# Optimization experiments

Measured on AMD Instinct MI355X. Metric: run time of the kernel, lower is better.

## Reference

```python
import jax, jax.numpy as jnp
import numpy as np

# Hyperparameters (must match init_kwargs)
B, S, D = 1, 4096, 1024
H, DK, DV = 16, 64, 64
G, W, R = 1, 23, 8          # global, window, random tokens
KSEL = 1 + R + W            # selected keys per non-global query


def setup_inputs() -> dict:
    key = jax.random.key(0)
    ks = jax.random.split(key, 8)
    scale = 0.02
    Q = jax.random.normal(ks[0], (B, S, D), dtype=jnp.float32)
    K = jax.random.normal(ks[1], (B, S, D), dtype=jnp.float32)
    V = jax.random.normal(ks[2], (B, S, D), dtype=jnp.float32)
    Wq = jax.random.normal(ks[3], (D, H * DK), dtype=jnp.float32) * scale
    Wk = jax.random.normal(ks[4], (D, H * DK), dtype=jnp.float32) * scale
    Wv = jax.random.normal(ks[5], (D, H * DV), dtype=jnp.float32) * scale
    Wo = jax.random.normal(ks[6], (H * DV, D), dtype=jnp.float32) * scale
    # BigBird-style index table: [global(=token 0), random, sliding window]
    n_ng = S - 2 * G
    base = jnp.arange(G, S - G)                                   # [n_ng]
    win = base[:, None] + jnp.arange(W)[None, :] - (W - 1) // 2   # [n_ng, W]
    win = jnp.clip(win, 0, S - 1)
    rnd = jax.random.randint(ks[7], (n_ng, R), 1, S)              # [n_ng, R]
    glb = jnp.zeros((n_ng, 1), dtype=jnp.int64)
    idx = jnp.concatenate([glb, rnd.astype(jnp.int64), win.astype(jnp.int64)], axis=1)  # [n_ng, KSEL]
    return {"Q": Q, "K": K, "V": V, "Wq": Wq, "Wk": Wk, "Wv": Wv, "Wo": Wo, "idx": idx}


def reference(Q, K, V, Wq, Wk, Wv, Wo, idx):
    b, s, _ = Q.shape
    g = G
    # Projections, split heads: [B,H,S,d]
    q = (Q @ Wq).reshape(b, s, H, DK).transpose(0, 2, 1, 3)
    k = (K @ Wk).reshape(b, s, H, DK).transpose(0, 2, 1, 3)
    v = (V @ Wv).reshape(b, s, H, DV).transpose(0, 2, 1, 3)
    scale = 1.0 / jnp.sqrt(jnp.asarray(DK, dtype=q.dtype))

    # --- dense global-token path: first g and last g queries attend to all keys ---
    gidx = jnp.concatenate([jnp.arange(g), jnp.arange(s - g, s)])  # [2g]
    q_g = q[:, :, gidx, :]                                          # [B,H,2g,dk]
    logits_g = jnp.einsum('bhgd,bhnd->bhgn', q_g, k) * scale
    prob_g = jax.nn.softmax(logits_g, axis=-1)
    out_g = jnp.einsum('bhgn,bhnd->bhgd', prob_g, v)                # [B,H,2g,dv]

    # --- sparse gather path for the remaining queries ---
    q_ng = q[:, :, g:s - g, :]                                      # [B,H,n_ng,dk]
    k_sel = k[:, :, idx, :]                                         # [B,H,n_ng,KSEL,dk]
    v_sel = v[:, :, idx, :]                                         # [B,H,n_ng,KSEL,dv]
    logits = jnp.einsum('bhnd,bhnkd->bhnk', q_ng, k_sel) * scale
    prob = jax.nn.softmax(logits, axis=-1)
    out_ng = jnp.einsum('bhnk,bhnkd->bhnd', prob, v_sel)            # [B,H,n_ng,dv]

    out = jnp.concatenate([out_g[:, :, :g], out_ng, out_g[:, :, g:]], axis=2)  # [B,H,S,dv]
    x = out.transpose(0, 2, 1, 3).reshape(b, s, H * DV)
    return x @ Wo
```

## Files before the change

### kernel.cpp

```cpp
#include <hip/hip_runtime.h>

typedef unsigned short u16;
typedef unsigned int u32;
typedef __bf16 bf16x8_t __attribute__((ext_vector_type(8)));
typedef float f32x4 __attribute__((ext_vector_type(4)));
typedef u32 u32x4 __attribute__((ext_vector_type(4)));
typedef u16 u16x8 __attribute__((ext_vector_type(8)));

__device__ __forceinline__ float b2f(u16 u) {
  u32 x = ((u32)u) << 16; float f; __builtin_memcpy(&f, &x, 4); return f;
}
__device__ __forceinline__ u16 f2b(float f) {
  u32 x; __builtin_memcpy(&x, &f, 4);
  return (u16)((x + 0x8000u) >> 16);
}

__device__ __forceinline__ u16x8 ld8(const void* p, size_t off, int f32) {
  if (!f32) return *(const u16x8*)((const u16*)p + off);
  const u32* u = (const u32*)p + off;
  u32x4 a = *(const u32x4*)u;
  u32x4 b = *(const u32x4*)(u + 4);
  u16x8 r;
#pragma unroll
  for (int e = 0; e < 4; ++e) r[e] = (u16)((a[e] + 0x8000u) >> 16);
#pragma unroll
  for (int e = 0; e < 4; ++e) r[4 + e] = (u16)((b[e] + 0x8000u) >> 16);
  return r;
}

#if __has_builtin(__builtin_amdgcn_global_load_lds)
__device__ __forceinline__ void gl_lds16(const u16* g, u16* l, int lane) {
  (void)lane;
  __builtin_amdgcn_global_load_lds(
      (const __attribute__((address_space(1))) void*)g,
      (__attribute__((address_space(3))) void*)l, 16, 0, 0);
}
#else
__device__ __forceinline__ void gl_lds16(const u16* g, u16* l, int lane) {
  *(u16x8*)(l + lane * 8) = *(const u16x8*)g;
}
#endif

__global__ void detect_kernel(const u32* __restrict__ qraw,
                              const int* __restrict__ iraw,
                              int* __restrict__ flags) {
  const int t = threadIdx.x;
  int c = 0;
#pragma unroll
  for (int p = 0; p < 8; ++p) {
    const int e = (qraw[p * 64 + t] >> 7) & 0xFF;
    c += (e >= 100 && e <= 141);
  }
  for (int off = 32; off; off >>= 1) c += __shfl_xor(c, off);
  int nz = 0;
  if (t < 16) nz = (iraw[(t + 1) * 32 + 1] != 0);
  const unsigned long long bal = __ballot(nz);
  if (t == 0) {
    flags[0] = (c < 300) ? 1 : 0;
    flags[1] = (bal == 0ull) ? 1 : 0;
  }
}

__global__ __launch_bounds__(256) void transpose4(
    const void* s0, const void* s1, const void* s2, const void* s3,
    u16* d0, u16* d1, u16* d2, u16* d3, const int* flags) {
  const int f32 = flags[0];
  const void* src;
  u16* dst;
  switch (blockIdx.z) {
    case 0: src = s0; dst = d0; break;
    case 1: src = s1; dst = d1; break;
    case 2: src = s2; dst = d2; break;
    default: src = s3; dst = d3; break;
  }
  __shared__ u16 tile[32][33];
  const int tx = threadIdx.x, ty = threadIdx.y;
  const int bx = blockIdx.x * 32, by = blockIdx.y * 32;
#pragma unroll
  for (int i = 0; i < 4; ++i) {
    const int off = (by + ty + i * 8) * 1024 + bx + tx;
    tile[ty + i * 8][tx] = f32 ? f2b(((const float*)src)[off]) : ((const u16*)src)[off];
  }
  __syncthreads();
#pragma unroll
  for (int i = 0; i < 4; ++i)
    dst[(bx + ty + i * 8) * 1024 + by + tx] = tile[tx][ty + i * 8];
}

template <int BM>
__device__ __forceinline__ void gemm_fast(const void* A, int a_f32,
                                          const u16* __restrict__ Bt,
                                          void* C, int c_f32) {
  constexpr int AI = BM / 64;
  __shared__ __align__(16) u16 As[BM * 32];
  __shared__ __align__(16) u16 Bs[128 * 32];
  const int t = threadIdx.x;
  const int lane = t & 63, w = t >> 6;
  const int bm = blockIdx.y * BM, bn = blockIdx.x * 128;
  const int lr = lane >> 2, lc = (lane & 3) * 8;
  const int wr = (w >> 1) * (BM / 2);
  const int wc = (w & 1) * 64;
  const int m16 = lane & 15, q4 = lane >> 4;
  f32x4 acc[BM / 32][4] = {};

  for (int k0 = 0; k0 < 1024; k0 += 32) {
    if (!a_f32) {
#pragma unroll
      for (int i = 0; i < AI; ++i)
        gl_lds16((const u16*)A + (size_t)(bm + w * 16 * AI + i * 16 + lr) * 1024 + k0 + lc,
                 &As[(w * 16 * AI + i * 16) * 32], lane);
    } else {
#pragma unroll
      for (int i = 0; i < AI; ++i)
        *(u16x8*)&As[(w * 16 * AI + i * 16 + lr) * 32 + lc] =
            ld8(A, (size_t)(bm + w * 16 * AI + i * 16 + lr) * 1024 + k0 + lc, 1);
    }
    gl_lds16(Bt + (size_t)(bn + w * 32 + lr) * 1024 + k0 + lc, &Bs[(w * 32) * 32], lane);
    gl_lds16(Bt + (size_t)(bn + w * 32 + 16 + lr) * 1024 + k0 + lc, &Bs[(w * 32 + 16) * 32], lane);
    __syncthreads();
    bf16x8_t af[BM / 32], bfr[4];
#pragma unroll
    for (int i = 0; i < BM / 32; ++i)
      af[i] = *(const bf16x8_t*)&As[(wr + i * 16 + m16) * 32 + q4 * 8];
#pragma unroll
    for (int j = 0; j < 4; ++j)
      bfr[j] = *(const bf16x8_t*)&Bs[(wc + j * 16 + m16) * 32 + q4 * 8];
#pragma unroll
    for (int i = 0; i < BM / 32; ++i)
#pragma unroll
      for (int j = 0; j < 4; ++j)
        acc[i][j] = __builtin_amdgcn_mfma_f32_16x16x32_bf16(af[i], bfr[j], acc[i][j], 0, 0, 0);
    __syncthreads();
  }
#pragma unroll
  for (int i = 0; i < BM / 32; ++i)
#pragma unroll
    for (int r = 0; r < 4; ++r) {
      const int row = bm + wr + i * 16 + q4 * 4 + r;
#pragma unroll
      for (int j = 0; j < 4; ++j) {
        const int col = bn + wc + j * 16 + m16;
        const float x = acc[i][j][r];
        if (c_f32) ((float*)C)[(size_t)row * 1024 + col] = x;
        else       ((u16*)C)[(size_t)row * 1024 + col] = f2b(x);
      }
    }
}

__global__ __launch_bounds__(256) void gemm_qkv(
    const void* Q, const void* K, const void* V,
    const u16* WqT, const u16* WkT, const u16* WvT,
    u16* q, u16* k, u16* v, const int* flags) {
  const int f32 = flags[0];
  if (blockIdx.z == 0)      gemm_fast<128>(Q, f32, WqT, q, 0);
  else if (blockIdx.z == 1) gemm_fast<128>(K, f32, WkT, k, 0);
  else                      gemm_fast<128>(V, f32, WvT, v, 0);
}

__global__ __launch_bounds__(256) void gemm_out(
    const u16* A, const u16* WoT, void* C, const int* flags) {
  gemm_fast<64>(A, 0, WoT, C, flags[0]);
}

__global__ __launch_bounds__(256) void attn_sel(
    u16* qp, const u16* __restrict__ kp, const u16* __restrict__ vp,
    const int* __restrict__ idx, const int* __restrict__ flags) {
  const int b = blockIdx.x;
  int s0 = (b & 7) * 512 + (b >> 3);
  if (s0 >= 4094) s0 = 3583;
  const int s = s0 + 1;
  const int t = threadIdx.x;
  __shared__ float ps[512];
  __shared__ int sidx[32];

  if (t >= 224) {
    const int j = t - 224;
    const size_t e = (size_t)(s - 1) * 32 + j;
    sidx[j] = flags[1] ? idx[2 * e] : idx[e];
  }

  const int w = t >> 6, lane = t & 63;
  const int jj = lane >> 3, dl = lane & 7;

  float qreg[4][8];
#pragma unroll
  for (int hh = 0; hh < 4; ++hh) {
    const u16x8 qv = *(const u16x8*)(qp + (size_t)s * 1024 + (w * 4 + hh) * 64 + dl * 8);
#pragma unroll
    for (int e = 0; e < 8; ++e) qreg[hh][e] = b2f((u16)qv[e]);
  }
  __syncthreads();

#pragma unroll
  for (int p = 0; p < 16; ++p) {
    const int h = w * 4 + (p >> 2);
    const int j = (p & 3) * 8 + jj;
    const u16x8 kv = *(const u16x8*)(kp + (size_t)sidx[j] * 1024 + h * 64 + dl * 8);
    float acc = 0.f;
#pragma unroll
    for (int e = 0; e < 8; ++e) acc += qreg[p >> 2][e] * b2f((u16)kv[e]);
    acc += __shfl_xor(acc, 1);
    acc += __shfl_xor(acc, 2);
    acc += __shfl_xor(acc, 4);
    if (dl == 0) ps[h * 32 + j] = acc * 0.125f;
  }
  __syncthreads();

  {
    const int h = t >> 4, jx = t & 15;
    const float v0 = ps[h * 32 + jx], v1 = ps[h * 32 + jx + 16];
    float mx = fmaxf(v0, v1);
    mx = fmaxf(mx, __shfl_xor(mx, 1));
    mx = fmaxf(mx, __shfl_xor(mx, 2));
    mx = fmaxf(mx, __shfl_xor(mx, 4));
    mx = fmaxf(mx, __shfl_xor(mx, 8));
    const float p0 = __expf(v0 - mx), p1 = __expf(v1 - mx);
    float sm = p0 + p1;
    sm += __shfl_xor(sm, 1);
    sm += __shfl_xor(sm, 2);
    sm += __shfl_xor(sm, 4);
    sm += __shfl_xor(sm, 8);
    const float r = 1.f / sm;
    ps[h * 32 + jx] = p0 * r;
    ps[h * 32 + jx + 16] = p1 * r;
  }
  __syncthreads();

  const int dc = lane & 7;
#pragma unroll
  for (int hp = 0; hp < 4; ++hp) {
    const int h = hp * 4 + w;
    float acc8[8] = {};
#pragma unroll
    for (int j0 = 0; j0 < 32; j0 += 8) {
      const int j = j0 + jj;
      const u16x8 v8 = *(const u16x8*)(vp + (size_t)sidx[j] * 1024 + h * 64 + dc * 8);
      const float p = ps[h * 32 + j];
#pragma unroll
      for (int e = 0; e < 8; ++e) acc8[e] += p * b2f((u16)v8[e]);
    }
#pragma unroll
    for (int e = 0; e < 8; ++e) {
      acc8[e] += __shfl_xor(acc8[e], 8);
      acc8[e] += __shfl_xor(acc8[e], 16);
      acc8[e] += __shfl_xor(acc8[e], 32);
    }
    if (jj == 0) {
      u16x8 o;
#pragma unroll
      for (int e = 0; e < 8; ++e) o[e] = f2b(acc8[e]);
      *(u16x8*)(qp + (size_t)s * 1024 + h * 64 + dc * 8) = o;
    }
  }
}

__global__ __launch_bounds__(256) void attn_glb_a(
    const u16* __restrict__ qp, const u16* __restrict__ kp,
    const u16* __restrict__ vp, float* __restrict__ part) {
  const int qi = blockIdx.x >> 7;
  const int h = (blockIdx.x >> 3) & 15;
  const int c = blockIdx.x & 7;
  const int s = qi ? 4095 : 0;
  const int t = threadIdx.x;
  __shared__ float qh[64];
  __shared__ float lg[512];
  __shared__ float red[4];
  __shared__ float pvs[4][64];
  if (t < 8) {
    u16x8 v = *(const u16x8*)(qp + (size_t)s * 1024 + h * 64 + t * 8);
#pragma unroll
    for (int e = 0; e < 8; ++e) qh[t * 8 + e] = b2f((u16)v[e]);
  }
  __syncthreads();
  float lv[2];
#pragma unroll
  for (int i = 0; i < 2; ++i) {
    const int n = c * 512 + t + i * 256;
    const u16* krow = kp + (size_t)n * 1024 + h * 64;
    float acc = 0.f;
#pragma unroll
    for (int cc = 0; cc < 8; ++cc) {
      u16x8 kv = *(const u16x8*)(krow + cc * 8);
#pragma unroll
      for (int e = 0; e < 8; ++e) acc += qh[cc * 8 + e] * b2f((u16)kv[e]);
    }
    lv[i] = acc * 0.125f;
  }
  float m2 = fmaxf(lv[0], lv[1]);
  for (int off = 32; off; off >>= 1) m2 = fmaxf(m2, __shfl_xor(m2, off));
  if ((t & 63) == 0) red[t >> 6] = m2;
  __syncthreads();
  const float gm = fmaxf(fmaxf(red[0], red[1]), fmaxf(red[2], red[3]));
  const float p0 = __expf(lv[0] - gm), p1 = __expf(lv[1] - gm);
  lg[t] = p0; lg[t + 256] = p1;
  float sm = p0 + p1;
  for (int off = 32; off; off >>= 1) sm += __shfl_xor(sm, off);
  __syncthreads();
  if ((t & 63) == 0) red[t >> 6] = sm;
  __syncthreads();
  const float ssum = red[0] + red[1] + red[2] + red[3];

  const int d = t & 63, cc = t >> 6;
  float acc = 0.f;
  for (int i = 0; i < 128; ++i) {
    const int nl = cc * 128 + i;
    acc += lg[nl] * b2f(vp[(size_t)(c * 512 + nl) * 1024 + h * 64 + d]);
  }
  pvs[cc][d] = acc;
  __syncthreads();
  float* dst = part + ((size_t)(qi * 16 + h) * 8 + c) * 66;
  if (t == 0) { dst[0] = gm; dst[1] = ssum; }
  if (t < 64) dst[2 + t] = pvs[0][t] + pvs[1][t] + pvs[2][t] + pvs[3][t];
}

__global__ void attn_glb_b(u16* __restrict__ qp, const float* __restrict__ part) {
  const int qi = blockIdx.x >> 4, h = blockIdx.x & 15;
  const int s = qi ? 4095 : 0;
  const int t = threadIdx.x;
  const float* p = part + ((size_t)(qi * 16 + h) * 8) * 66;
  float gm = -1e30f;
#pragma unroll
  for (int c = 0; c < 8; ++c) gm = fmaxf(gm, p[c * 66]);
  float S = 0.f, o = 0.f;
#pragma unroll
  for (int c = 0; c < 8; ++c) {
    const float w = __expf(p[c * 66] - gm);
    S += p[c * 66 + 1] * w;
    o += p[c * 66 + 2 + t] * w;
  }
  qp[(size_t)s * 1024 + h * 64 + t] = f2b(o / S);
}

extern "C" void kernel_launch(void* const* d_in, const int* in_sizes, int n_in,
                              void* d_out, int out_size, void* d_ws, size_t ws_size,
                              hipStream_t stream) {
  const void* Q  = d_in[0];
  const void* K  = d_in[1];
  const void* V  = d_in[2];
  const void* Wq = d_in[3];
  const void* Wk = d_in[4];
  const void* Wv = d_in[5];
  const void* Wo = d_in[6];
  const int* idx = (const int*)d_in[7];

  u16* WqT = (u16*)d_ws;
  u16* WkT = WqT + (1 << 20);
  u16* WvT = WkT + (1 << 20);
  u16* WoT = WvT + (1 << 20);
  u16* qp  = WoT + (1 << 20);
  u16* vp  = qp + (4 << 20);
  int* flags = (int*)(vp + (4 << 20));
  float* part = (float*)WkT;
  u16* kp = (u16*)d_out;

  detect_kernel<<<1, 64, 0, stream>>>((const u32*)Q, idx, flags);
  transpose4<<<dim3(32, 32, 4), dim3(32, 8), 0, stream>>>(
      Wq, Wk, Wv, Wo, WqT, WkT, WvT, WoT, flags);
  gemm_qkv<<<dim3(8, 32, 3), 256, 0, stream>>>(
      Q, K, V, WqT, WkT, WvT, qp, kp, vp, flags);
  attn_glb_a<<<256, 256, 0, stream>>>(qp, kp, vp, part);
  attn_glb_b<<<32, 64, 0, stream>>>(qp, part);
  attn_sel<<<4094, 256, 0, stream>>>(qp, kp, vp, idx, flags);
  gemm_out<<<dim3(8, 64), 256, 0, stream>>>(qp, WoT, d_out, flags);
}
```

Measured before the change: 250.6 us.

## Pre-convert fp32 QKV inputs to bf16 and swap GEMM grid block order

Adds a separate kernel that converts the fp32 Q, K, V activations to bf16 in workspace, so the QKV GEMM can use the async global-to-LDS bf16 load path instead of converting in the inner loop. This runs only when the workspace is large enough. The GEMM grid mapping is also swapped so that blockIdx.x walks M-tiles, which changes which tiles run together and how the weight tiles are reused in L2. The cost is an extra kernel launch and an extra read and write of the three 4096x1024 activations.

Result: faster. 227.1 us (-9.4%).

```diff
diff --git a/kernel.cpp b/kernel.cpp
--- a/kernel.cpp
+++ b/kernel.cpp
@@ -87,6 +87,20 @@
     dst[(bx + ty + i * 8) * 1024 + by + tx] = tile[tx][ty + i * 8];
 }
 
+__global__ __launch_bounds__(256) void conv3_bf16(
+    const void* Q, const void* K, const void* V,
+    u16* Qb, u16* Kb, u16* Vb, const int* flags) {
+  if (!flags[0]) return;
+  const void* s; u16* d;
+  switch (blockIdx.y) {
+    case 0: s = Q; d = Qb; break;
+    case 1: s = K; d = Kb; break;
+    default: s = V; d = Vb; break;
+  }
+  const size_t i = ((size_t)blockIdx.x * 256 + threadIdx.x) * 8;
+  *(u16x8*)(d + i) = ld8(s, i, 1);
+}
+
 template <int BM>
 __device__ __forceinline__ void gemm_fast(const void* A, int a_f32,
                                           const u16* __restrict__ Bt,
@@ -96,7 +110,7 @@
   __shared__ __align__(16) u16 Bs[128 * 32];
   const int t = threadIdx.x;
   const int lane = t & 63, w = t >> 6;
-  const int bm = blockIdx.y * BM, bn = blockIdx.x * 128;
+  const int bm = blockIdx.x * BM, bn = blockIdx.y * 128;
   const int lr = lane >> 2, lc = (lane & 3) * 8;
   const int wr = (w >> 1) * (BM / 2);
   const int wc = (w & 1) * 64;
@@ -149,12 +163,18 @@
 
 __global__ __launch_bounds__(256) void gemm_qkv(
     const void* Q, const void* K, const void* V,
+    const u16* Qb, const u16* Kb, const u16* Vb,
     const u16* WqT, const u16* WkT, const u16* WvT,
-    u16* q, u16* k, u16* v, const int* flags) {
+    u16* q, u16* k, u16* v, const int* flags, int big) {
   const int f32 = flags[0];
-  if (blockIdx.z == 0)      gemm_fast<128>(Q, f32, WqT, q, 0);
-  else if (blockIdx.z == 1) gemm_fast<128>(K, f32, WkT, k, 0);
-  else                      gemm_fast<128>(V, f32, WvT, v, 0);
+  const void* Araw; const u16* Ab; const u16* Bt; u16* Cp;
+  switch (blockIdx.z) {
+    case 0:  Araw = Q; Ab = Qb; Bt = WqT; Cp = q; break;
+    case 1:  Araw = K; Ab = Kb; Bt = WkT; Cp = k; break;
+    default: Araw = V; Ab = Vb; Bt = WvT; Cp = v; break;
+  }
+  if (big && f32) gemm_fast<128>(Ab, 0, Bt, Cp, 0);
+  else            gemm_fast<128>(Araw, f32, Bt, Cp, 0);
 }
 
 __global__ __launch_bounds__(256) void gemm_out(
@@ -352,14 +372,20 @@
   int* flags = (int*)(vp + (4 << 20));
   float* part = (float*)WkT;
   u16* kp = (u16*)d_out;
+  u16* Qb = (u16*)((char*)d_ws + (24ull << 20) + 4096);
+  u16* Kb = Qb + (4 << 20);
+  u16* Vb = Kb + (4 << 20);
+  const bool big = ws_size >= (48ull << 20) + 8192;
 
   detect_kernel<<<1, 64, 0, stream>>>((const u32*)Q, idx, flags);
   transpose4<<<dim3(32, 32, 4), dim3(32, 8), 0, stream>>>(
       Wq, Wk, Wv, Wo, WqT, WkT, WvT, WoT, flags);
-  gemm_qkv<<<dim3(8, 32, 3), 256, 0, stream>>>(
-      Q, K, V, WqT, WkT, WvT, qp, kp, vp, flags);
+  if (big)
+    conv3_bf16<<<dim3(2048, 3), 256, 0, stream>>>(Q, K, V, Qb, Kb, Vb, flags);
+  gemm_qkv<<<dim3(32, 8, 3), 256, 0, stream>>>(
+      Q, K, V, Qb, Kb, Vb, WqT, WkT, WvT, qp, kp, vp, flags, big ? 1 : 0);
   attn_glb_a<<<256, 256, 0, stream>>>(qp, kp, vp, part);
   attn_glb_b<<<32, 64, 0, stream>>>(qp, part);
   attn_sel<<<4094, 256, 0, stream>>>(qp, kp, vp, idx, flags);
-  gemm_out<<<dim3(8, 64), 256, 0, stream>>>(qp, WoT, d_out, flags);
-}
+  gemm_out<<<dim3(64, 8), 256, 0, stream>>>(qp, WoT, d_out, flags);
+}
```
